# Kernel tuning notes

Hardware: AMD Instinct MI355X
Metric: run time of the kernel (lower is better)

The kernel has to match this reference:

```python
import jax, jax.numpy as jnp
import numpy as np

D_MODEL = 1024
N_HEADS = 16
D_HEAD = D_MODEL // N_HEADS
B, T = 4, 2048


def setup_inputs() -> dict:
    key = jax.random.key(0)
    ks = jax.random.split(key, 5)
    s = 1.0 / np.sqrt(D_MODEL)
    x = jax.random.normal(ks[0], (B, T, D_MODEL), dtype=jnp.float32)
    Wq = jax.random.uniform(ks[1], (D_MODEL, D_MODEL), jnp.float32, -s, s)
    Wk = jax.random.uniform(ks[2], (D_MODEL, D_MODEL), jnp.float32, -s, s)
    Wv = jax.random.uniform(ks[3], (D_MODEL, D_MODEL), jnp.float32, -s, s)
    Wo = jax.random.uniform(ks[4], (D_MODEL, D_MODEL), jnp.float32, -s, s)
    # causal mask, 0 = masked (matches torch masked_fill(mask == 0, -inf))
    mask = jnp.tril(jnp.ones((T, T), dtype=jnp.int32))[None, None, :, :]
    return {"x": x, "Wq": Wq, "Wk": Wk, "Wv": Wv, "Wo": Wo, "mask": mask}


def reference(x, Wq, Wk, Wv, Wo, mask):
    def split_heads(t):  # [B,T,D] -> [B,H,T,d]
        return t.reshape(B, T, N_HEADS, D_HEAD).transpose(0, 2, 1, 3)

    Q = split_heads(x @ Wq.T)
    K = split_heads(x @ Wk.T)
    V = split_heads(x @ Wv.T)
    scale = 1.0 / np.sqrt(D_HEAD).astype(np.float32)
    attn = jnp.einsum('bhqd,bhkd->bhqk', Q, K) * scale
    attn = jnp.where(mask == 0, -jnp.inf, attn)
    attn = jax.nn.softmax(attn, axis=-1)
    out = jnp.einsum('bhqk,bhkd->bhqd', attn, V)
    out = out.transpose(0, 2, 1, 3).reshape(B, T, D_MODEL)
    return out @ Wo.T
```

## Files before the change

kernel.cpp:

```cpp
#include <hip/hip_runtime.h>
#include <hip/hip_bf16.h>
#include <cstdint>

#define T_SEQ   2048
#define DMODEL  1024
#define NHEADS  16
#define DHEAD   64
#define B_SZ    4
#define M_ROWS  (B_SZ * T_SEQ)
#define QSCALE  0.1803368801111204f

typedef unsigned short u16;
typedef __attribute__((ext_vector_type(8))) __bf16 bf16x8;
typedef __attribute__((ext_vector_type(4))) float  f32x4;

__device__ __forceinline__ u16 f2bf(float f) {
  uint32_t u = __float_as_uint(f);
  u += 0x7FFF + ((u >> 16) & 1);
  return (u16)(u >> 16);
}

__device__ __forceinline__ float fast_exp2(float x) {
  return __builtin_amdgcn_exp2f(x);
}

__device__ __forceinline__ void gload_lds16(const void* g, void* l) {
  __builtin_amdgcn_global_load_lds(
      (const __attribute__((address_space(1))) void*)g,
      (__attribute__((address_space(3))) void*)l, 16, 0, 0);
}

__global__ void cvt_all(const float* __restrict__ x,  const float* __restrict__ Wq,
                        const float* __restrict__ Wk, const float* __restrict__ Wv,
                        const float* __restrict__ Wo, u16* __restrict__ xb,
                        u16* __restrict__ Wb) {
  const int NX = (B_SZ * T_SEQ * DMODEL) / 8;
  const int NW = (DMODEL * DMODEL) / 8;
  int i = blockIdx.x * blockDim.x + threadIdx.x;
  int stride = gridDim.x * blockDim.x;
  for (; i < NX + 4 * NW; i += stride) {
    const float* src; u16* dst; int idx;
    if (i < NX) { src = x; dst = xb; idx = i; }
    else {
      int j = i - NX, w = j >> 17;
      idx = j & (NW - 1);
      src = (w == 0) ? Wq : (w == 1) ? Wk : (w == 2) ? Wv : Wo;
      dst = Wb + (size_t)w * (DMODEL * DMODEL);
    }
    const float4* s4 = (const float4*)src;
    float4 a = s4[2 * idx], b = s4[2 * idx + 1];
    union { u16 u[8]; uint4 v; } o;
    o.u[0] = f2bf(a.x); o.u[1] = f2bf(a.y); o.u[2] = f2bf(a.z); o.u[3] = f2bf(a.w);
    o.u[4] = f2bf(b.x); o.u[5] = f2bf(b.y); o.u[6] = f2bf(b.z); o.u[7] = f2bf(b.w);
    ((uint4*)dst)[idx] = o.v;
  }
}

template <int MODE>
__global__ __launch_bounds__(256) void gemm3(
    const u16* __restrict__ A, const u16* __restrict__ Wall,
    float* __restrict__ C0, u16* __restrict__ Qb, u16* __restrict__ Kb,
    u16* __restrict__ Vtb) {
  constexpr int K = DMODEL;
  constexpr int NTILES = K / 64;
  constexpr int NT = (MODE == 0) ? 8 : 24;
  __shared__ u16 As[2][128 * 64];
  __shared__ u16 Bs[2][128 * 64];
  const int tid = threadIdx.x;
  const int wid = tid >> 6, lane = tid & 63;
  const int flat = blockIdx.x;
  const int xcd = flat & 7, serial = flat >> 3;
  const int tm = (serial / NT) * 8 + xcd;
  const int tn = serial % NT;
  const int wr = wid >> 1, wc = wid & 1;
  const int lrow = lane & 15, lq = lane >> 4;
  const int sr = lrow & 7;
  const int srow = lane >> 3;
  const int csw = ((lane & 7) ^ srow) * 8;

  const u16* Arow = A    + (size_t)(tm * 128 + srow) * K + csw;
  const u16* Wrow = Wall + (size_t)(tn * 128 + srow) * K + csw;

  auto stage = [&](int k0, int b) {
#pragma unroll
    for (int it = 0; it < 4; ++it) {
      int rbase = it * 32 + wid * 8;
      gload_lds16(Arow + (size_t)rbase * K + k0, &As[b][rbase * 64]);
      gload_lds16(Wrow + (size_t)rbase * K + k0, &Bs[b][rbase * 64]);
    }
  };

  f32x4 acc[4][4];
#pragma unroll
  for (int m = 0; m < 4; m++)
#pragma unroll
    for (int n = 0; n < 4; n++) acc[m][n] = f32x4{0.f, 0.f, 0.f, 0.f};

  auto compute = [&](int b) {
#pragma unroll
    for (int kk = 0; kk < 2; ++kk) {
      bf16x8 a[4], bb[4];
      const int co = ((kk * 4 + lq) ^ sr) * 8;
#pragma unroll
      for (int m = 0; m < 4; m++)
        a[m] = *(const bf16x8*)&As[b][(wr * 64 + m * 16 + lrow) * 64 + co];
#pragma unroll
      for (int n = 0; n < 4; n++)
        bb[n] = *(const bf16x8*)&Bs[b][(wc * 64 + n * 16 + lrow) * 64 + co];
#pragma unroll
      for (int m = 0; m < 4; m++)
#pragma unroll
        for (int n = 0; n < 4; n++)
          acc[m][n] = __builtin_amdgcn_mfma_f32_16x16x32_bf16(a[m], bb[n], acc[m][n], 0, 0, 0);
    }
  };

  stage(0, 0);
  stage(64, 1);
  asm volatile("s_waitcnt vmcnt(8)" ::: "memory");
  __builtin_amdgcn_s_barrier();

  for (int t = 0; t < NTILES; t += 2) {
    compute(0);
    asm volatile("" ::: "memory");
    __builtin_amdgcn_s_barrier();
    if (t + 2 < NTILES) {
      stage((t + 2) * 64, 0);
      asm volatile("s_waitcnt vmcnt(8)" ::: "memory");
    } else {
      asm volatile("s_waitcnt vmcnt(0)" ::: "memory");
    }
    __builtin_amdgcn_s_barrier();
    compute(1);
    if (t + 3 < NTILES) {
      asm volatile("" ::: "memory");
      __builtin_amdgcn_s_barrier();
      stage((t + 3) * 64, 1);
      asm volatile("s_waitcnt vmcnt(8)" ::: "memory");
      __builtin_amdgcn_s_barrier();
    }
  }

#pragma unroll
  for (int m = 0; m < 4; m++) {
#pragma unroll
    for (int n = 0; n < 4; n++) {
#pragma unroll
      for (int v = 0; v < 4; v++) {
        int i = tm * 128 + wr * 64 + m * 16 + lq * 4 + v;
        int j = tn * 128 + wc * 64 + n * 16 + lrow;
        if constexpr (MODE == 0) {
          C0[(size_t)i * DMODEL + j] = acc[m][n][v];
        } else {
          int y = j >> 10, jj = j & 1023;
          float val = acc[m][n][v] * (y == 0 ? QSCALE : 1.0f);
          int b_ = i >> 11, t_ = i & 2047, h_ = jj >> 6, d_ = jj & 63;
          if (y == 2)
            Vtb[((size_t)(b_ * NHEADS + h_) * 64 + d_) * T_SEQ + t_] = f2bf(val);
          else
            ((y == 0) ? Qb : Kb)[((size_t)(b_ * NHEADS + h_) * T_SEQ + t_) * 64 + d_] = f2bf(val);
        }
      }
    }
  }
}

__global__ __launch_bounds__(256) void flash_attn(
    const u16* __restrict__ Q, const u16* __restrict__ Kg,
    const u16* __restrict__ Vt, u16* __restrict__ Ao) {
  __shared__ u16 Ks[2][64 * 64];
  __shared__ u16 Vs[2][64 * 64];
  __shared__ u16 Ps[4][16 * 64];
  const int tid = threadIdx.x, wid = tid >> 6, lane = tid & 63;
  const int flat = blockIdx.x;
  const int serial = flat >> 3;
  const int bh = (serial >> 4) * 8 + (flat & 7);
  const int qi = serial & 15;
  const int qtA = qi, qtB = 31 - qi;
  const int lrow = lane & 15, lq = lane >> 4;
  const int sr = lrow & 7;
  const int srow = lane >> 3;
  const int csw = ((lane & 7) ^ srow) * 8;

  const u16* qbase = Q + ((size_t)bh * T_SEQ + wid * 16 + lrow) * 64 + lq * 8;
  const bf16x8 qA0 = *(const bf16x8*)(qbase + (size_t)qtA * 4096);
  const bf16x8 qA1 = *(const bf16x8*)(qbase + (size_t)qtA * 4096 + 32);
  const bf16x8 qB0 = *(const bf16x8*)(qbase + (size_t)qtB * 4096);
  const bf16x8 qB1 = *(const bf16x8*)(qbase + (size_t)qtB * 4096 + 32);

  bf16x8 ones;
  {
    union { u16 u; __bf16 b; } c; c.u = 0x3F80;
#pragma unroll
    for (int j = 0; j < 8; j++) ones[j] = c.b;
  }

  f32x4 poA[4], poB[4], lA, lB;
#pragma unroll
  for (int n = 0; n < 4; n++) { poA[n] = f32x4{0.f,0.f,0.f,0.f}; poB[n] = f32x4{0.f,0.f,0.f,0.f}; }
  lA = f32x4{0.f,0.f,0.f,0.f}; lB = f32x4{0.f,0.f,0.f,0.f};

  auto stage = [&](int kt, int b) {
#pragma unroll
    for (int it = 0; it < 2; ++it) {
      int rbase = it * 32 + wid * 8;
      gload_lds16(Kg + ((size_t)bh * T_SEQ + kt * 64 + rbase + srow) * 64 + csw,
                  &Ks[b][rbase * 64]);
      gload_lds16(Vt + ((size_t)bh * 64 + rbase + srow) * T_SEQ + kt * 64 + csw,
                  &Vs[b][rbase * 64]);
    }
  };

  stage(0, 0);
  __syncthreads();
  int cur = 0;

  for (int kt = 0; kt <= qtB; ++kt) {
    if (kt < qtB) stage(kt + 1, cur ^ 1);

    bf16x8 kf0[4], kf1[4];
#pragma unroll
    for (int n = 0; n < 4; n++) {
      kf0[n] = *(const bf16x8*)&Ks[cur][(n * 16 + lrow) * 64 + ((lq ^ sr) * 8)];
      kf1[n] = *(const bf16x8*)&Ks[cur][(n * 16 + lrow) * 64 + (((lq + 4) ^ sr) * 8)];
    }

    auto apply = [&](const bf16x8& q0, const bf16x8& q1,
                     f32x4 (&po)[4], f32x4& l4, bool diag) {
      f32x4 s[4];
#pragma unroll
      for (int n = 0; n < 4; n++) {
        f32x4 a = f32x4{0.f, 0.f, 0.f, 0.f};
        a = __builtin_amdgcn_mfma_f32_16x16x32_bf16(q0, kf0[n], a, 0, 0, 0);
        a = __builtin_amdgcn_mfma_f32_16x16x32_bf16(q1, kf1[n], a, 0, 0, 0);
        s[n] = a;
      }
      if (diag) {
#pragma unroll
        for (int n = 0; n < 4; n++)
#pragma unroll
          for (int v = 0; v < 4; v++) {
            int kcol = n * 16 + lrow;
            int qrow = wid * 16 + lq * 4 + v;
            if (kcol > qrow) s[n][v] = -1e30f;
          }
      }
#pragma unroll
      for (int n = 0; n < 4; n++)
#pragma unroll
        for (int v = 0; v < 4; v++) {
          float p = fast_exp2(s[n][v]);
          int col = n * 16 + lrow;
          int r = lq * 4 + v;
          Ps[wid][r * 64 + (((col >> 3) ^ (r & 7)) * 8) + (col & 7)] =
              (u16)(__float_as_uint(p) >> 16);
        }
#pragma unroll
      for (int kk = 0; kk < 2; kk++) {
        bf16x8 pa = *(const bf16x8*)&Ps[wid][lrow * 64 + (((kk * 4 + lq) ^ sr) * 8)];
#pragma unroll
        for (int n = 0; n < 4; n++) {
          bf16x8 vf = *(const bf16x8*)&Vs[cur][(n * 16 + lrow) * 64 + (((kk * 4 + lq) ^ sr) * 8)];
          po[n] = __builtin_amdgcn_mfma_f32_16x16x32_bf16(pa, vf, po[n], 0, 0, 0);
        }
        l4 = __builtin_amdgcn_mfma_f32_16x16x32_bf16(pa, ones, l4, 0, 0, 0);
      }
    };

    if (kt <= qtA) apply(qA0, qA1, poA, lA, kt == qtA);
    apply(qB0, qB1, poB, lB, kt == qtB);

    asm volatile("s_waitcnt vmcnt(0)" ::: "memory");
    __syncthreads();
    cur ^= 1;
  }

  const int b_ = bh >> 4, h_ = bh & 15;
  auto epi = [&](int qt_, f32x4 (&po)[4], f32x4& l4) {
    float rl[4];
#pragma unroll
    for (int v = 0; v < 4; v++) rl[v] = 1.0f / l4[v];
#pragma unroll
    for (int n = 0; n < 4; n++)
#pragma unroll
      for (int v = 0; v < 4; v++) {
        int t_ = qt_ * 64 + wid * 16 + lq * 4 + v;
        int col = h_ * 64 + n * 16 + lrow;
        Ao[((size_t)b_ * T_SEQ + t_) * DMODEL + col] = f2bf(po[n][v] * rl[v]);
      }
  };
  epi(qtA, poA, lA);
  epi(qtB, poB, lB);
}

extern "C" void kernel_launch(void* const* d_in, const int* in_sizes, int n_in,
                              void* d_out, int out_size, void* d_ws, size_t ws_size,
                              hipStream_t stream) {
  const float* x  = (const float*)d_in[0];
  const float* Wq = (const float*)d_in[1];
  const float* Wk = (const float*)d_in[2];
  const float* Wv = (const float*)d_in[3];
  const float* Wo = (const float*)d_in[4];
  float* out = (float*)d_out;

  char* ws = (char*)d_ws;
  u16* xb  = (u16*)(ws);
  u16* Wb  = (u16*)(ws + 16777216);
  u16* Qb  = (u16*)(ws + 25165824);
  u16* Kb  = (u16*)(ws + 41943040);
  u16* Vtb = (u16*)(ws + 58720256);
  u16* Aob = xb;

  cvt_all<<<2048, 256, 0, stream>>>(x, Wq, Wk, Wv, Wo, xb, Wb);

  gemm3<1><<<1536, 256, 0, stream>>>(xb, Wb, nullptr, Qb, Kb, Vtb);

  flash_attn<<<1024, 256, 0, stream>>>(Qb, Kb, Vtb, Aob);

  gemm3<0><<<512, 256, 0, stream>>>(Aob, Wb + 3 * 1048576, out, nullptr, nullptr, nullptr);
}
```

Before: 194.2 us.

## Replace QKV projection GEMM with 256x256-tile 8-wave ping-pong kernel

Adds a dedicated QKV projection kernel that uses 256x256 output tiles, 512 threads (8 waves) and double-buffered LDS split into halves. Each K-step is broken into four MFMA quadrants interleaved with staged global-to-LDS loads, barriers and s_setprio, so loads and math overlap across waves. The larger tile raises arithmetic intensity and halves the block count versus the old 128x128 template. The cost is much higher LDS and register use, and a fragile hand-written waitcnt and barrier schedule. The output GEMM is de-templated but otherwise unchanged.

New measurement: 193.0 us. About the same (-0.6%).

```diff
diff --git a/kernel.cpp b/kernel.cpp
--- a/kernel.cpp
+++ b/kernel.cpp
@@ -29,6 +29,13 @@
       (const __attribute__((address_space(1))) void*)g,
       (__attribute__((address_space(3))) void*)l, 16, 0, 0);
 }
+
+#define BAR  __builtin_amdgcn_s_barrier()
+#define LG0  asm volatile("s_waitcnt lgkmcnt(0)" ::: "memory")
+#define VM4  asm volatile("s_waitcnt vmcnt(4)" ::: "memory")
+#define VM0  asm volatile("s_waitcnt vmcnt(0)" ::: "memory")
+#define PRIO1 __builtin_amdgcn_s_setprio(1)
+#define PRIO0 __builtin_amdgcn_s_setprio(0)
 
 __global__ void cvt_all(const float* __restrict__ x,  const float* __restrict__ Wq,
                         const float* __restrict__ Wk, const float* __restrict__ Wv,
@@ -56,14 +63,133 @@
   }
 }
 
-template <int MODE>
+__global__ __launch_bounds__(512, 2) void gemm8p_qkv(
+    const u16* __restrict__ A, const u16* __restrict__ Wall,
+    u16* __restrict__ Qb, u16* __restrict__ Kb, u16* __restrict__ Vtb) {
+  constexpr int K = DMODEL;
+  __shared__ u16 As[2][2][128 * 64];
+  __shared__ u16 Bs[2][2][128 * 64];
+  const int tid = threadIdx.x;
+  const int wid = tid >> 6, lane = tid & 63;
+  const int wr = wid >> 2, wc = wid & 3;
+  const int flat = blockIdx.x;
+  const int xcd = flat & 7, serial = flat >> 3;
+  const int tm = (serial / 12) * 8 + xcd;
+  const int tn = serial % 12;
+  const int lrow = lane & 15, lq = lane >> 4;
+  const int sr = lrow & 7;
+  const int srow = tid >> 3;
+  const int csw = ((tid & 7) ^ (srow & 7)) * 8;
+  const int cha = (tid & 7) * 8;
+
+  const u16* Arow = A    + (size_t)(tm * 256 + srow) * K + csw;
+  const u16* Wrow = Wall + (size_t)(tn * 256 + srow) * K + csw;
+
+  auto stageA = [&](int kt, int d, int h) {
+    gload_lds16(Arow + (size_t)(h * 128) * K + kt,      &As[d][h][srow * 64 + cha]);
+    gload_lds16(Arow + (size_t)(h * 128 + 64) * K + kt, &As[d][h][(64 + srow) * 64 + cha]);
+  };
+  auto stageB = [&](int kt, int d, int h) {
+    gload_lds16(Wrow + (size_t)(h * 128) * K + kt,      &Bs[d][h][srow * 64 + cha]);
+    gload_lds16(Wrow + (size_t)(h * 128 + 64) * K + kt, &Bs[d][h][(64 + srow) * 64 + cha]);
+  };
+
+  f32x4 acc[8][4];
+#pragma unroll
+  for (int m = 0; m < 8; m++)
+#pragma unroll
+    for (int n = 0; n < 4; n++) acc[m][n] = f32x4{0.f, 0.f, 0.f, 0.f};
+
+  auto ldA = [&](bf16x8 (&a)[4][2], int d, int mb) {
+#pragma unroll
+    for (int m = 0; m < 4; m++)
+#pragma unroll
+      for (int kk = 0; kk < 2; kk++)
+        a[m][kk] = *(const bf16x8*)&As[d][wr][((mb + m) * 16 + lrow) * 64 + (((kk * 4 + lq) ^ sr) * 8)];
+  };
+  auto ldB = [&](bf16x8 (&b)[2][2], int d, int nb) {
+#pragma unroll
+    for (int n = 0; n < 2; n++)
+#pragma unroll
+      for (int kk = 0; kk < 2; kk++)
+        b[n][kk] = *(const bf16x8*)&Bs[d][wc >> 1][((wc & 1) * 64 + (nb + n) * 16 + lrow) * 64 + (((kk * 4 + lq) ^ sr) * 8)];
+  };
+  auto quad = [&](bf16x8 (&a)[4][2], bf16x8 (&b)[2][2], int mb, int nb) {
+#pragma unroll
+    for (int m = 0; m < 4; m++)
+#pragma unroll
+      for (int n = 0; n < 2; n++)
+#pragma unroll
+        for (int kk = 0; kk < 2; kk++)
+          acc[mb + m][nb + n] =
+              __builtin_amdgcn_mfma_f32_16x16x32_bf16(a[m][kk], b[n][kk], acc[mb + m][nb + n], 0, 0, 0);
+  };
+
+  stageB(0, 0, 0); stageB(0, 0, 1);
+  stageA(0, 0, 0); stageA(0, 0, 1);
+  stageB(64, 1, 0); stageB(64, 1, 1);
+  VM4;
+  BAR;
+
+#pragma unroll
+  for (int i = 0; i < 8; ++i) {
+    const int t1 = 2 * i + 1, u0 = 2 * i + 2, u1 = 2 * i + 3;
+    bf16x8 aq0[4][2], aq1[4][2], bq0[2][2], bq1[2][2];
+    ldA(aq0, 0, 0); ldB(bq0, 0, 0);
+    stageA(t1 * 64, 1, 0);
+    BAR; LG0; PRIO1; quad(aq0, bq0, 0, 0); PRIO0; BAR;
+    ldB(bq1, 0, 2);
+    stageA(t1 * 64, 1, 1);
+    BAR; LG0; PRIO1; quad(aq0, bq1, 0, 2); PRIO0; BAR;
+    ldA(aq1, 0, 4);
+    if (u0 < 16) stageB(u0 * 64, 0, 0);
+    BAR; LG0; PRIO1; quad(aq1, bq1, 4, 2); PRIO0; BAR;
+    if (u0 < 16) stageB(u0 * 64, 0, 1);
+    BAR; PRIO1; quad(aq1, bq0, 4, 0); PRIO0;
+    if (i < 7) { VM4; } else { VM0; }
+    BAR;
+    ldA(aq0, 1, 0); ldB(bq0, 1, 0);
+    if (u0 < 16) stageA(u0 * 64, 0, 0);
+    BAR; LG0; PRIO1; quad(aq0, bq0, 0, 0); PRIO0; BAR;
+    ldB(bq1, 1, 2);
+    if (u0 < 16) stageA(u0 * 64, 0, 1);
+    BAR; LG0; PRIO1; quad(aq0, bq1, 0, 2); PRIO0; BAR;
+    ldA(aq1, 1, 4);
+    if (u1 < 16) stageB(u1 * 64, 1, 0);
+    BAR; LG0; PRIO1; quad(aq1, bq1, 4, 2); PRIO0; BAR;
+    if (u1 < 16) stageB(u1 * 64, 1, 1);
+    BAR; PRIO1; quad(aq1, bq0, 4, 0); PRIO0;
+    if (i < 7) { VM4; }
+    BAR;
+  }
+
+  const int y = tn >> 2;
+  const int hcol = (tn & 3) * 4 + wc;
+  u16* dst = (y == 0) ? Qb : (y == 1) ? Kb : Vtb;
+  const float scale = (y == 0) ? QSCALE : 1.0f;
+#pragma unroll
+  for (int m = 0; m < 8; m++)
+#pragma unroll
+    for (int n = 0; n < 4; n++)
+#pragma unroll
+      for (int v = 0; v < 4; v++) {
+        int i_ = tm * 256 + wr * 128 + m * 16 + lq * 4 + v;
+        int d_ = n * 16 + lrow;
+        int b_ = i_ >> 11, t_ = i_ & 2047;
+        float val = acc[m][n][v] * scale;
+        if (y == 2)
+          dst[((size_t)(b_ * NHEADS + hcol) * 64 + d_) * T_SEQ + t_] = f2bf(val);
+        else
+          dst[((size_t)(b_ * NHEADS + hcol) * T_SEQ + t_) * 64 + d_] = f2bf(val);
+      }
+}
+
 __global__ __launch_bounds__(256) void gemm3(
     const u16* __restrict__ A, const u16* __restrict__ Wall,
-    float* __restrict__ C0, u16* __restrict__ Qb, u16* __restrict__ Kb,
-    u16* __restrict__ Vtb) {
+    float* __restrict__ C0) {
   constexpr int K = DMODEL;
   constexpr int NTILES = K / 64;
-  constexpr int NT = (MODE == 0) ? 8 : 24;
+  constexpr int NT = 8;
   __shared__ u16 As[2][128 * 64];
   __shared__ u16 Bs[2][128 * 64];
   const int tid = threadIdx.x;
@@ -142,27 +268,15 @@
   }
 
 #pragma unroll
-  for (int m = 0; m < 4; m++) {
-#pragma unroll
-    for (int n = 0; n < 4; n++) {
+  for (int m = 0; m < 4; m++)
+#pragma unroll
+    for (int n = 0; n < 4; n++)
 #pragma unroll
       for (int v = 0; v < 4; v++) {
         int i = tm * 128 + wr * 64 + m * 16 + lq * 4 + v;
         int j = tn * 128 + wc * 64 + n * 16 + lrow;
-        if constexpr (MODE == 0) {
-          C0[(size_t)i * DMODEL + j] = acc[m][n][v];
-        } else {
-          int y = j >> 10, jj = j & 1023;
-          float val = acc[m][n][v] * (y == 0 ? QSCALE : 1.0f);
-          int b_ = i >> 11, t_ = i & 2047, h_ = jj >> 6, d_ = jj & 63;
-          if (y == 2)
-            Vtb[((size_t)(b_ * NHEADS + h_) * 64 + d_) * T_SEQ + t_] = f2bf(val);
-          else
-            ((y == 0) ? Qb : Kb)[((size_t)(b_ * NHEADS + h_) * T_SEQ + t_) * 64 + d_] = f2bf(val);
-        }
-      }
-    }
-  }
+        C0[(size_t)i * DMODEL + j] = acc[m][n][v];
+      }
 }
 
 __global__ __launch_bounds__(256) void flash_attn(
@@ -313,9 +427,9 @@
 
   cvt_all<<<2048, 256, 0, stream>>>(x, Wq, Wk, Wv, Wo, xb, Wb);
 
-  gemm3<1><<<1536, 256, 0, stream>>>(xb, Wb, nullptr, Qb, Kb, Vtb);
+  gemm8p_qkv<<<384, 512, 0, stream>>>(xb, Wb, Qb, Kb, Vtb);
 
   flash_attn<<<1024, 256, 0, stream>>>(Qb, Kb, Vtb, Aob);
 
-  gemm3<0><<<512, 256, 0, stream>>>(Aob, Wb + 3 * 1048576, out, nullptr, nullptr, nullptr);
-}
+  gemm3<<<512, 256, 0, stream>>>(Aob, Wb + 3 * 1048576, out);
+}
```

## Replace QKV GEMM with 256x192-tile 8-wave ping-pong pipelined kernel

Applied to the files above, without the earlier changes.

Adds a dedicated QKV projection kernel that uses 512-thread blocks with 256x192 output tiles, so 512 blocks cover the fused QKV output instead of 1536 blocks with 128x128 tiles. Its loop is an 8-wave schedule that interleaves LDS fragment loads, async global-to-LDS staging and MFMA clusters, separated by barriers and raised wave priority. The aim is more operand reuse per tile and better overlap of memory and compute. In exchange it needs much more LDS and registers per block, which limits occupancy, and it adds many barriers. The output-projection GEMM is simplified to a non-templated version.

Measured after the change: 198.8 us. 1.02x slower.

```diff
diff --git a/kernel.cpp b/kernel.cpp
--- a/kernel.cpp
+++ b/kernel.cpp
@@ -29,6 +29,13 @@
       (const __attribute__((address_space(1))) void*)g,
       (__attribute__((address_space(3))) void*)l, 16, 0, 0);
 }
+
+#define BAR  __builtin_amdgcn_s_barrier()
+#define LG0  asm volatile("s_waitcnt lgkmcnt(0)" ::: "memory")
+#define VM3  asm volatile("s_waitcnt vmcnt(3)" ::: "memory")
+#define VM0  asm volatile("s_waitcnt vmcnt(0)" ::: "memory")
+#define PRIO1 __builtin_amdgcn_s_setprio(1)
+#define PRIO0 __builtin_amdgcn_s_setprio(0)
 
 __global__ void cvt_all(const float* __restrict__ x,  const float* __restrict__ Wq,
                         const float* __restrict__ Wk, const float* __restrict__ Wv,
@@ -56,14 +63,126 @@
   }
 }
 
-template <int MODE>
+__global__ __launch_bounds__(512, 2) void gemm8p_qkv(
+    const u16* __restrict__ A, const u16* __restrict__ Wall,
+    u16* __restrict__ Qb, u16* __restrict__ Kb, u16* __restrict__ Vtb) {
+  constexpr int K = DMODEL;
+  __shared__ u16 As[2][256 * 64];
+  __shared__ u16 Bs[2][192 * 64];
+  const int tid = threadIdx.x;
+  const int wid = tid >> 6, lane = tid & 63;
+  const int wr = wid >> 2, wc = wid & 3;
+  const int flat = blockIdx.x;
+  const int xcd = flat & 7, serial = flat >> 3;
+  const int tm = (serial >> 4) * 8 + xcd;
+  const int tn = serial & 15;
+  const int lrow = lane & 15, lq = lane >> 4;
+  const int sr = lrow & 7;
+  const int srow = tid >> 3;
+  const int csw = ((tid & 7) ^ (srow & 7)) * 8;
+  const int cha = (tid & 7) * 8;
+
+  const u16* Arow = A    + (size_t)(tm * 256 + srow) * K + csw;
+  const u16* Brow = Wall + (size_t)(tn * 192 + srow) * K + csw;
+
+  auto stageAu = [&](int kt, int d, int u) {
+    gload_lds16(Arow + (size_t)(u * 64) * K + kt, &As[d][(u * 64 + srow) * 64 + cha]);
+  };
+  auto stageBu = [&](int kt, int d, int u) {
+    gload_lds16(Brow + (size_t)(u * 64) * K + kt, &Bs[d][(u * 64 + srow) * 64 + cha]);
+  };
+
+  f32x4 acc[8][3];
+#pragma unroll
+  for (int m = 0; m < 8; m++)
+#pragma unroll
+    for (int n = 0; n < 3; n++) acc[m][n] = f32x4{0.f, 0.f, 0.f, 0.f};
+
+  auto ldA = [&](bf16x8 (&a)[4], int d, int mb, int kk) {
+#pragma unroll
+    for (int m = 0; m < 4; m++)
+      a[m] = *(const bf16x8*)&As[d][(wr * 128 + (mb + m) * 16 + lrow) * 64 + (((kk * 4 + lq) ^ sr) * 8)];
+  };
+  auto ldB = [&](bf16x8 (&b)[3], int d, int kk) {
+#pragma unroll
+    for (int n = 0; n < 3; n++)
+      b[n] = *(const bf16x8*)&Bs[d][(wc * 48 + n * 16 + lrow) * 64 + (((kk * 4 + lq) ^ sr) * 8)];
+  };
+  auto cl = [&](bf16x8 (&a)[4], bf16x8 (&b)[3], int mb) {
+#pragma unroll
+    for (int m = 0; m < 4; m++)
+#pragma unroll
+      for (int n = 0; n < 3; n++)
+        acc[mb + m][n] = __builtin_amdgcn_mfma_f32_16x16x32_bf16(a[m], b[n], acc[mb + m][n], 0, 0, 0);
+  };
+
+  stageAu(0, 0, 0); stageAu(0, 0, 1); stageAu(0, 0, 2); stageAu(0, 0, 3);
+  stageBu(0, 0, 0); stageBu(0, 0, 1); stageBu(0, 0, 2);
+  stageBu(64, 1, 0); stageBu(64, 1, 1); stageBu(64, 1, 2);
+  VM3;
+  BAR;
+
+#pragma unroll
+  for (int i = 0; i < 8; ++i) {
+    const int t1k = (2 * i + 1) * 64;
+    const int u0 = 2 * i + 2, u1 = 2 * i + 3;
+    const int u0k = u0 * 64, u1k = u1 * 64;
+    bf16x8 aqA[4], aqB[4], bq0[3], bq1[3];
+    ldA(aqA, 0, 0, 0); ldB(bq0, 0, 0);
+    stageAu(t1k, 1, 0); stageAu(t1k, 1, 1);
+    BAR; LG0; PRIO1; cl(aqA, bq0, 0); PRIO0; BAR;
+    ldA(aqB, 0, 0, 1); ldB(bq1, 0, 1);
+    stageAu(t1k, 1, 2); stageAu(t1k, 1, 3);
+    BAR; LG0; PRIO1; cl(aqB, bq1, 0); PRIO0; BAR;
+    ldA(aqA, 0, 4, 1);
+    if (u0 < 16) { stageBu(u0k, 0, 0); stageBu(u0k, 0, 1); }
+    BAR; LG0; PRIO1; cl(aqA, bq1, 4); PRIO0; BAR;
+    ldA(aqB, 0, 4, 0);
+    if (u0 < 16) stageBu(u0k, 0, 2);
+    BAR; LG0; PRIO1; cl(aqB, bq0, 4); PRIO0;
+    if (i < 7) { VM3; } else { VM0; }
+    BAR;
+    ldA(aqA, 1, 0, 0); ldB(bq0, 1, 0);
+    if (u0 < 16) { stageAu(u0k, 0, 0); stageAu(u0k, 0, 1); }
+    BAR; LG0; PRIO1; cl(aqA, bq0, 0); PRIO0; BAR;
+    ldA(aqB, 1, 0, 1); ldB(bq1, 1, 1);
+    if (u0 < 16) { stageAu(u0k, 0, 2); stageAu(u0k, 0, 3); }
+    BAR; LG0; PRIO1; cl(aqB, bq1, 0); PRIO0; BAR;
+    ldA(aqA, 1, 4, 1);
+    if (u1 < 16) { stageBu(u1k, 1, 0); stageBu(u1k, 1, 1); }
+    BAR; LG0; PRIO1; cl(aqA, bq1, 4); PRIO0; BAR;
+    ldA(aqB, 1, 4, 0);
+    if (u1 < 16) stageBu(u1k, 1, 2);
+    BAR; LG0; PRIO1; cl(aqB, bq0, 4); PRIO0;
+    if (i < 7) { VM3; }
+    BAR;
+  }
+
+#pragma unroll
+  for (int m = 0; m < 8; m++)
+#pragma unroll
+    for (int n = 0; n < 3; n++)
+#pragma unroll
+      for (int v = 0; v < 4; v++) {
+        int i_ = tm * 256 + wr * 128 + m * 16 + lq * 4 + v;
+        int j  = tn * 192 + wc * 48 + n * 16 + lrow;
+        int y = j >> 10, jj = j & 1023;
+        int h_ = jj >> 6, d_ = jj & 63;
+        int b_ = i_ >> 11, t_ = i_ & 2047;
+        float val = acc[m][n][v] * (y == 0 ? QSCALE : 1.0f);
+        if (y == 2)
+          Vtb[((size_t)(b_ * NHEADS + h_) * 64 + d_) * T_SEQ + t_] = f2bf(val);
+        else
+          ((y == 0) ? Qb : Kb)[((size_t)(b_ * NHEADS + h_) * T_SEQ + t_) * 64 + d_] = f2bf(val);
+      }
+}
+
 __global__ __launch_bounds__(256) void gemm3(
     const u16* __restrict__ A, const u16* __restrict__ Wall,
-    float* __restrict__ C0, u16* __restrict__ Qb, u16* __restrict__ Kb,
-    u16* __restrict__ Vtb) {
+    float* __restrict__ C0) {
   constexpr int K = DMODEL;
   constexpr int NTILES = K / 64;
-  constexpr int NT = (MODE == 0) ? 8 : 24;
+  constexpr int NT = 8;
   __shared__ u16 As[2][128 * 64];
   __shared__ u16 Bs[2][128 * 64];
   const int tid = threadIdx.x;
@@ -142,27 +261,15 @@
   }
 
 #pragma unroll
-  for (int m = 0; m < 4; m++) {
-#pragma unroll
-    for (int n = 0; n < 4; n++) {
+  for (int m = 0; m < 4; m++)
+#pragma unroll
+    for (int n = 0; n < 4; n++)
 #pragma unroll
       for (int v = 0; v < 4; v++) {
         int i = tm * 128 + wr * 64 + m * 16 + lq * 4 + v;
         int j = tn * 128 + wc * 64 + n * 16 + lrow;
-        if constexpr (MODE == 0) {
-          C0[(size_t)i * DMODEL + j] = acc[m][n][v];
-        } else {
-          int y = j >> 10, jj = j & 1023;
-          float val = acc[m][n][v] * (y == 0 ? QSCALE : 1.0f);
-          int b_ = i >> 11, t_ = i & 2047, h_ = jj >> 6, d_ = jj & 63;
-          if (y == 2)
-            Vtb[((size_t)(b_ * NHEADS + h_) * 64 + d_) * T_SEQ + t_] = f2bf(val);
-          else
-            ((y == 0) ? Qb : Kb)[((size_t)(b_ * NHEADS + h_) * T_SEQ + t_) * 64 + d_] = f2bf(val);
-        }
-      }
-    }
-  }
+        C0[(size_t)i * DMODEL + j] = acc[m][n][v];
+      }
 }
 
 __global__ __launch_bounds__(256) void flash_attn(
@@ -313,9 +420,9 @@
 
   cvt_all<<<2048, 256, 0, stream>>>(x, Wq, Wk, Wv, Wo, xb, Wb);
 
-  gemm3<1><<<1536, 256, 0, stream>>>(xb, Wb, nullptr, Qb, Kb, Vtb);
+  gemm8p_qkv<<<512, 512, 0, stream>>>(xb, Wb, Qb, Kb, Vtb);
 
   flash_attn<<<1024, 256, 0, stream>>>(Qb, Kb, Vtb, Aob);
 
-  gemm3<0><<<512, 256, 0, stream>>>(Aob, Wb + 3 * 1048576, out, nullptr, nullptr, nullptr);
-}
+  gemm3<<<512, 256, 0, stream>>>(Aob, Wb + 3 * 1048576, out);
+}
```
